# Optimization experiments

Hardware: AMD Instinct MI355X
Metric: run time of the kernel (lower is better)

## Reference

```python
import jax, jax.numpy as jnp
import numpy as np


def setup_inputs() -> dict:
    key = jax.random.key(0)
    k1, k2 = jax.random.split(key)
    B, R1, R2, D = 16, 2048, 2048, 256
    matrix_1 = jax.random.normal(k1, (B, R1, D), dtype=jnp.float32)
    matrix_2 = jax.random.normal(k2, (B, R2, D), dtype=jnp.float32)
    return {"matrix_1": matrix_1, "matrix_2": matrix_2}


def reference(matrix_1, matrix_2):
    # Original keras layer tiles matrix_1 to [B, R1, R2, D] and matrix_2 to
    # [B, R1, R2, D], then applies the dot-product similarity (elementwise
    # multiply + sum over last dim). That is exactly a batched matmul:
    #   scores[b, i, j] = sum_d matrix_1[b, i, d] * matrix_2[b, j, d]
    return jnp.einsum('bid,bjd->bij', matrix_1, matrix_2)
```

## Files before the change

kernel.cpp:

```cpp
#include <hip/hip_runtime.h>
#include <hip/hip_bf16.h>
#include <stdint.h>


typedef __bf16 bf16x8 __attribute__((ext_vector_type(8)));
typedef __bf16 bf16x4 __attribute__((ext_vector_type(4)));
typedef float f32x4 __attribute__((ext_vector_type(4)));

#define NB 16
#define DM 2048
#define DN 2048
#define DK 256
#define BM 128
#define BN 128
#define BK 32
#define NT (DK / BK)
#define NWG (NB * (DM/BM) * (DN/BN))

__global__ __launch_bounds__(256) void fused_gemm(const float* __restrict__ A,
                                                  const float* __restrict__ B,
                                                  float* __restrict__ C) {
    __shared__ __bf16 As[2][BM * BK];
    __shared__ __bf16 Bs[2][BN * BK];

    const int t = threadIdx.x;

    const int bid = blockIdx.x;
    const int swz = (bid & 7) * (NWG / 8) + (bid >> 3);
    const int b    = swz >> 8;
    const int rem  = swz & 255;
    const int brow = (rem >> 4) << 7;
    const int bcol = (rem & 15) << 7;

    const float* At = A + (size_t)b * DM * DK + (size_t)brow * DK;
    const float* Bt = B + (size_t)b * DN * DK + (size_t)bcol * DK;

    const int w    = t >> 6;
    const int l    = t & 63;
    const int wr   = (w >> 1) * 64;
    const int wc   = (w & 1) * 64;
    const int lrow = l & 15;
    const int lko  = (l >> 4) * 8;

    f32x4 acc[4][4] = {};

    float4 va[4], vb[4];

    auto issue_loads = [&](int kt) {
#pragma unroll
        for (int i = 0; i < 4; ++i) {
            const int c = t + i * 256;
            const int r = c >> 3, q = c & 7;
            va[i] = *reinterpret_cast<const float4*>(At + (size_t)r * DK + kt * BK + q * 4);
            vb[i] = *reinterpret_cast<const float4*>(Bt + (size_t)r * DK + kt * BK + q * 4);
        }
    };
    auto write_lds = [&](int buf) {
#pragma unroll
        for (int i = 0; i < 4; ++i) {
            const int c = t + i * 256;
            const int r = c >> 3, q = c & 7;
            bf16x4 ha = { (__bf16)va[i].x, (__bf16)va[i].y, (__bf16)va[i].z, (__bf16)va[i].w };
            bf16x4 hb = { (__bf16)vb[i].x, (__bf16)vb[i].y, (__bf16)vb[i].z, (__bf16)vb[i].w };
            *reinterpret_cast<bf16x4*>(&As[buf][r * BK + q * 4]) = ha;
            *reinterpret_cast<bf16x4*>(&Bs[buf][r * BK + q * 4]) = hb;
        }
    };

    issue_loads(0);
    write_lds(0);
    __syncthreads();

    int cur = 0;
#pragma unroll 1
    for (int kt = 0; kt < NT; ++kt) {
        if (kt + 1 < NT) issue_loads(kt + 1);

        bf16x8 af[4], bfr[4];
#pragma unroll
        for (int m = 0; m < 4; ++m)
            af[m] = *reinterpret_cast<const bf16x8*>(&As[cur][(wr + m * 16 + lrow) * BK + lko]);
#pragma unroll
        for (int n = 0; n < 4; ++n)
            bfr[n] = *reinterpret_cast<const bf16x8*>(&Bs[cur][(wc + n * 16 + lrow) * BK + lko]);
#pragma unroll
        for (int m = 0; m < 4; ++m)
#pragma unroll
            for (int n = 0; n < 4; ++n)
                acc[m][n] = __builtin_amdgcn_mfma_f32_16x16x32_bf16(af[m], bfr[n], acc[m][n], 0, 0, 0);

        if (kt + 1 < NT) write_lds(cur ^ 1);
        __syncthreads();
        cur ^= 1;
    }

    float* Cb = C + (size_t)b * DM * DN;
    const int crow = brow + wr + (l >> 4) * 4;
    const int ccol = bcol + wc + lrow;
#pragma unroll
    for (int m = 0; m < 4; ++m)
#pragma unroll
        for (int j = 0; j < 4; ++j) {
            float* rowp = Cb + (size_t)(crow + m * 16 + j) * DN + ccol;
#pragma unroll
            for (int n = 0; n < 4; ++n)
                __builtin_nontemporal_store(acc[m][n][j], rowp + n * 16);
        }
}

extern "C" void kernel_launch(void* const* d_in, const int* in_sizes, int n_in,
                              void* d_out, int out_size, void* d_ws, size_t ws_size,
                              hipStream_t stream) {
    const float* m1 = (const float*)d_in[0];
    const float* m2 = (const float*)d_in[1];
    float* out = (float*)d_out;
    (void)d_ws; (void)ws_size;

    fused_gemm<<<NWG, 256, 0, stream>>>(m1, m2, out);
}
```

Measured before the change: 81.62 us.

## Load MFMA fragments directly from global memory, dropping LDS staging, use fp16

Removes shared-memory staging and barriers: each lane loads its own MFMA operand fragments straight from global memory, converts them to fp16 with packed round-toward-zero, and feeds f16 MFMAs. The K loop is fully unrolled and launch bounds request two blocks per CU. This drops LDS writes, reads and syncthreads, but each wave now reads its own rows from global memory, so data reuse falls to the L1/L2 caches and global traffic per block rises. fp16 also has less range than bf16, which the normal inputs tolerate.

```diff
diff --git a/kernel.cpp b/kernel.cpp
--- a/kernel.cpp
+++ b/kernel.cpp
@@ -3,8 +3,8 @@
 #include <stdint.h>
 
 
-typedef __bf16 bf16x8 __attribute__((ext_vector_type(8)));
-typedef __bf16 bf16x4 __attribute__((ext_vector_type(4)));
+typedef _Float16 f16x8 __attribute__((ext_vector_type(8)));
+typedef _Float16 f16x2 __attribute__((ext_vector_type(2)));
 typedef float f32x4 __attribute__((ext_vector_type(4)));
 
 #define NB 16
@@ -17,12 +17,9 @@
 #define NT (DK / BK)
 #define NWG (NB * (DM/BM) * (DN/BN))
 
-__global__ __launch_bounds__(256) void fused_gemm(const float* __restrict__ A,
-                                                  const float* __restrict__ B,
-                                                  float* __restrict__ C) {
-    __shared__ __bf16 As[2][BM * BK];
-    __shared__ __bf16 Bs[2][BN * BK];
-
+__global__ __launch_bounds__(256, 2) void fused_gemm(const float* __restrict__ A,
+                                                     const float* __restrict__ B,
+                                                     float* __restrict__ C) {
     const int t = threadIdx.x;
 
     const int bid = blockIdx.x;
@@ -32,9 +29,6 @@
     const int brow = (rem >> 4) << 7;
     const int bcol = (rem & 15) << 7;
 
-    const float* At = A + (size_t)b * DM * DK + (size_t)brow * DK;
-    const float* Bt = B + (size_t)b * DN * DK + (size_t)bcol * DK;
-
     const int w    = t >> 6;
     const int l    = t & 63;
     const int wr   = (w >> 1) * 64;
@@ -42,56 +36,48 @@
     const int lrow = l & 15;
     const int lko  = (l >> 4) * 8;
 
+    const float* Ab = A + (size_t)b * DM * DK + (size_t)(brow + wr + lrow) * DK + lko;
+    const float* Bb = B + (size_t)b * DN * DK + (size_t)(bcol + wc + lrow) * DK + lko;
+
     f32x4 acc[4][4] = {};
 
-    float4 va[4], vb[4];
-
-    auto issue_loads = [&](int kt) {
-#pragma unroll
-        for (int i = 0; i < 4; ++i) {
-            const int c = t + i * 256;
-            const int r = c >> 3, q = c & 7;
-            va[i] = *reinterpret_cast<const float4*>(At + (size_t)r * DK + kt * BK + q * 4);
-            vb[i] = *reinterpret_cast<const float4*>(Bt + (size_t)r * DK + kt * BK + q * 4);
-        }
-    };
-    auto write_lds = [&](int buf) {
-#pragma unroll
-        for (int i = 0; i < 4; ++i) {
-            const int c = t + i * 256;
-            const int r = c >> 3, q = c & 7;
-            bf16x4 ha = { (__bf16)va[i].x, (__bf16)va[i].y, (__bf16)va[i].z, (__bf16)va[i].w };
-            bf16x4 hb = { (__bf16)vb[i].x, (__bf16)vb[i].y, (__bf16)vb[i].z, (__bf16)vb[i].w };
-            *reinterpret_cast<bf16x4*>(&As[buf][r * BK + q * 4]) = ha;
-            *reinterpret_cast<bf16x4*>(&Bs[buf][r * BK + q * 4]) = hb;
-        }
+    auto cvt8 = [](const float4& lo, const float4& hi) -> f16x8 {
+        f16x2 p0 = __builtin_bit_cast(f16x2, __builtin_amdgcn_cvt_pkrtz(lo.x, lo.y));
+        f16x2 p1 = __builtin_bit_cast(f16x2, __builtin_amdgcn_cvt_pkrtz(lo.z, lo.w));
+        f16x2 p2 = __builtin_bit_cast(f16x2, __builtin_amdgcn_cvt_pkrtz(hi.x, hi.y));
+        f16x2 p3 = __builtin_bit_cast(f16x2, __builtin_amdgcn_cvt_pkrtz(hi.z, hi.w));
+        return f16x8{ p0[0], p0[1], p1[0], p1[1], p2[0], p2[1], p3[0], p3[1] };
     };
 
-    issue_loads(0);
-    write_lds(0);
-    __syncthreads();
+#pragma unroll
+    for (int kt = 0; kt < NT; ++kt) {
+        const int k0 = kt * BK;
 
-    int cur = 0;
-#pragma unroll 1
-    for (int kt = 0; kt < NT; ++kt) {
-        if (kt + 1 < NT) issue_loads(kt + 1);
+        float4 alo[4], ahi[4], blo[4], bhi[4];
+#pragma unroll
+        for (int m = 0; m < 4; ++m) {
+            const float* p = Ab + (size_t)(m * 16) * DK + k0;
+            alo[m] = *reinterpret_cast<const float4*>(p);
+            ahi[m] = *reinterpret_cast<const float4*>(p + 4);
+        }
+#pragma unroll
+        for (int n = 0; n < 4; ++n) {
+            const float* p = Bb + (size_t)(n * 16) * DK + k0;
+            blo[n] = *reinterpret_cast<const float4*>(p);
+            bhi[n] = *reinterpret_cast<const float4*>(p + 4);
+        }
 
-        bf16x8 af[4], bfr[4];
+        f16x8 af[4], bf[4];
 #pragma unroll
-        for (int m = 0; m < 4; ++m)
-            af[m] = *reinterpret_cast<const bf16x8*>(&As[cur][(wr + m * 16 + lrow) * BK + lko]);
+        for (int m = 0; m < 4; ++m) af[m] = cvt8(alo[m], ahi[m]);
 #pragma unroll
-        for (int n = 0; n < 4; ++n)
-            bfr[n] = *reinterpret_cast<const bf16x8*>(&Bs[cur][(wc + n * 16 + lrow) * BK + lko]);
+        for (int n = 0; n < 4; ++n) bf[n] = cvt8(blo[n], bhi[n]);
+
 #pragma unroll
         for (int m = 0; m < 4; ++m)
 #pragma unroll
             for (int n = 0; n < 4; ++n)
-                acc[m][n] = __builtin_amdgcn_mfma_f32_16x16x32_bf16(af[m], bfr[n], acc[m][n], 0, 0, 0);
-
-        if (kt + 1 < NT) write_lds(cur ^ 1);
-        __syncthreads();
-        cur ^= 1;
+                acc[m][n] = __builtin_amdgcn_mfma_f32_16x16x32_f16(af[m], bf[n], acc[m][n], 0, 0, 0);
     }
 
     float* Cb = C + (size_t)b * DM * DN;
```

Measured after the change: 264.7 us. 3.24x slower.
